# Performance work log

Measured on AMD Instinct MI355X. Metric: run time of the kernel, lower is better.

## Reference

```python
import jax, jax.numpy as jnp
import numpy as np
from jax import lax

EPS = 1e-5
F_IN, F_OUT, R = 128, 256, 16
B, H, W = 16, 128, 128


def _conv(x, w, stride):
    # x: [B,C,H,W], w: [O,I,kh,kw]; ME convs keep coordinates -> SAME padding
    return lax.conv_general_dilated(x, w, (stride, stride), 'SAME',
                                    dimension_numbers=('NCHW', 'OIHW', 'NCHW'))


def _bn(x, g, b, m, v):
    scale = g * lax.rsqrt(v + EPS)
    return x * scale[None, :, None, None] + (b - m * scale)[None, :, None, None]


def setup_inputs() -> dict:
    key = jax.random.key(0)
    ks = jax.random.split(key, 12)
    d = {}
    d['x'] = jax.random.normal(ks[0], (B, F_IN, H, W), jnp.float32)
    # BatchNorm params (eval mode running stats)
    d['bn1_g'] = jax.random.uniform(ks[1], (F_IN,), jnp.float32, 0.5, 1.5)
    d['bn1_b'] = jax.random.normal(ks[2], (F_IN,), jnp.float32) * 0.1
    d['bn1_m'] = jax.random.normal(ks[3], (F_IN,), jnp.float32) * 0.1
    d['bn1_v'] = jax.random.uniform(ks[4], (F_IN,), jnp.float32, 0.5, 1.5)
    d['bn2_g'] = jax.random.uniform(ks[5], (F_OUT,), jnp.float32, 0.5, 1.5)
    d['bn2_b'] = jax.random.normal(ks[6], (F_OUT,), jnp.float32) * 0.1
    d['bn2_m'] = jax.random.normal(ks[7], (F_OUT,), jnp.float32) * 0.1
    d['bn2_v'] = jax.random.uniform(ks[8], (F_OUT,), jnp.float32, 0.5, 1.5)
    # Conv weights (no bias, ME default)
    d['w_conv1'] = jax.random.normal(ks[9], (F_OUT, F_IN, 3, 3), jnp.float32) * (1.0 / np.sqrt(9 * F_IN))
    d['w_conv2'] = jax.random.normal(ks[10], (F_OUT, F_OUT, 3, 3), jnp.float32) * (1.0 / np.sqrt(9 * F_OUT))
    d['w_res'] = jax.random.normal(ks[11], (F_OUT, F_IN, 1, 1), jnp.float32) * (1.0 / np.sqrt(F_IN))
    # SE block linears
    k12, k13, k14, k15 = jax.random.split(jax.random.fold_in(key, 1), 4)
    d['se_w1'] = jax.random.normal(k12, (F_OUT // R, F_OUT), jnp.float32) * (1.0 / np.sqrt(F_OUT))
    d['se_b1'] = jax.random.normal(k13, (F_OUT // R,), jnp.float32) * 0.01
    d['se_w2'] = jax.random.normal(k14, (F_OUT, F_OUT // R), jnp.float32) * (1.0 / np.sqrt(F_OUT // R))
    d['se_b2'] = jax.random.normal(k15, (F_OUT,), jnp.float32) * 0.01
    return d


def reference(x, bn1_g, bn1_b, bn1_m, bn1_v, bn2_g, bn2_b, bn2_m, bn2_v,
              w_conv1, w_conv2, w_res, se_w1, se_b1, se_w2, se_b2):
    # shared BN+ReLU prefix (self.first_batch / self.first_relu reused)
    pre = jax.nn.relu(_bn(x, bn1_g, bn1_b, bn1_m, bn1_v))
    # residual branch: 1x1 stride-2 conv (f_out > f_in)
    residual = _conv(pre, w_res, 2)
    # main branch
    h = _conv(pre, w_conv1, 2)                          # [B,F_OUT,H/2,W/2]
    h = jax.nn.relu(_bn(h, bn2_g, bn2_b, bn2_m, bn2_v))
    h = _conv(h, w_conv2, 1)
    # SE attention: global avg pool -> FC -> ReLU -> FC -> sigmoid -> scale
    s = jnp.mean(h, axis=(2, 3))                        # [B,F_OUT]
    a = jax.nn.sigmoid(jax.nn.relu(s @ se_w1.T + se_b1) @ se_w2.T + se_b2)
    h = h * a[:, :, None, None]
    return h + residual
```

## Files before the change

### kernel.cpp

```cpp
#include <hip/hip_runtime.h>

typedef unsigned short u16;
typedef __attribute__((ext_vector_type(8))) unsigned short u16x8;
typedef __attribute__((ext_vector_type(8))) __bf16 bf16x8;
typedef __attribute__((ext_vector_type(4))) float f32x4;

__device__ __forceinline__ float bf2f(u16 u) {
    return __uint_as_float(((unsigned)u) << 16);
}
__device__ __forceinline__ u16 f2bf(float f) {
    unsigned u = __float_as_uint(f);
    return (u16)((u + 0x7FFFu + ((u >> 16) & 1u)) >> 16);
}

__global__ void setup_kernel(const float* __restrict__ w1, const float* __restrict__ w2,
                             const float* __restrict__ wr,
                             const float* __restrict__ g2, const float* __restrict__ b2,
                             const float* __restrict__ m2, const float* __restrict__ v2,
                             u16* __restrict__ w1t, u16* __restrict__ w2t,
                             u16* __restrict__ wrt, float* __restrict__ bias2f,
                             u16* __restrict__ pre, u16* __restrict__ h1) {
    int b = blockIdx.x;
    if (b < 3585) {
        int i = b * 256 + threadIdx.x;
        if (i < 294912) {
            int ci = i & 127; int t = i >> 7; int o = t & 255; int tap = t >> 8;
            int dy = tap / 3, dx = tap - dy * 3;
            float sc = g2[o] * rsqrtf(v2[o] + 1e-5f);
            w1t[i] = f2bf(w1[((o * 128 + ci) * 3 + dy) * 3 + dx] * sc);
        } else if (i < 294912 + 589824) {
            int j = i - 294912;
            int ci = j & 255; int t = j >> 8; int o = t & 255; int tap = t >> 8;
            int dy = tap / 3, dx = tap - dy * 3;
            w2t[j] = f2bf(w2[((o * 256 + ci) * 3 + dy) * 3 + dx]);
        } else if (i < 294912 + 589824 + 32768) {
            int j = i - (294912 + 589824);
            int ci = j & 127; int o = j >> 7;
            wrt[j] = f2bf(wr[o * 128 + ci]);
        } else {
            int o = i - (294912 + 589824 + 32768);
            if (o < 256) {
                float sc = g2[o] * rsqrtf(v2[o] + 1e-5f);
                bias2f[o] = b2[o] - m2[o] * sc;
            }
        }
    } else if (b < 3585 + 2056) {
        int i = (b - 3585) * 256 + threadIdx.x;
        if (i < 16 * 129 * 128) {
            int c = i & 127; int t = i >> 7; int n = t / 129; int xx = t - n * 129;
            pre[((n * 129 + 128) * 129 + xx) * 128 + c] = 0;
        } else {
            int j = i - 16 * 129 * 128;
            int c = j & 127; int t = j >> 7; int n = t >> 7; int y = t & 127;
            pre[((n * 129 + y) * 129 + 128) * 128 + c] = 0;
        }
    } else {
        int i = (b - (3585 + 2056)) * 256 + threadIdx.x;
        int c = i & 255;
        int t = i >> 8;
        int n = t / 260;
        int cl = t - n * 260;
        int y, x;
        if (cl < 66)       { y = 0;  x = cl; }
        else if (cl < 132) { y = 65; x = cl - 66; }
        else if (cl < 196) { x = 0;  y = cl - 131; }
        else               { x = 65; y = cl - 195; }
        h1[((n * 66 + y) * 66 + x) * 256 + c] = 0;
    }
}

__global__ void pre_kernel(const float* __restrict__ x, const float* __restrict__ g,
                           const float* __restrict__ b, const float* __restrict__ m,
                           const float* __restrict__ v, u16* __restrict__ pre) {
    __shared__ u16 tile[128 * 136];
    int n = blockIdx.x >> 7, y = blockIdx.x & 127;
    int tid = threadIdx.x;
    int c = tid >> 1, xh = (tid & 1) << 6;
    float sc = g[c] * rsqrtf(v[c] + 1e-5f);
    float bi = b[c] - m[c] * sc;
    const float4* src = (const float4*)(x + (((n * 128 + c) * 128 + y) << 7) + xh);
#pragma unroll
    for (int j = 0; j < 16; ++j) {
        float4 val = src[j];
        int xb = xh + j * 4;
        tile[(xb + 0) * 136 + c] = f2bf(fmaxf(val.x * sc + bi, 0.f));
        tile[(xb + 1) * 136 + c] = f2bf(fmaxf(val.y * sc + bi, 0.f));
        tile[(xb + 2) * 136 + c] = f2bf(fmaxf(val.z * sc + bi, 0.f));
        tile[(xb + 3) * 136 + c] = f2bf(fmaxf(val.w * sc + bi, 0.f));
    }
    __syncthreads();
    int c0 = (tid & 15) << 3;
#pragma unroll
    for (int xi = 0; xi < 8; ++xi) {
        int xx = xi * 16 + (tid >> 4);
        u16x8 val = *(const u16x8*)&tile[xx * 136 + c0];
        *(u16x8*)(pre + ((n * 129 + y) * 129 + xx) * 128 + c0) = val;
    }
}

template <int CIN, int NTAPS, int STRIDE, bool BIASRELU, bool POOL>
__global__ __launch_bounds__(512, 2)
void conv_8ph(const u16* __restrict__ in, const u16* __restrict__ wt,
              const float* __restrict__ bias, u16* __restrict__ out,
              float* __restrict__ pool_out,
              int in_row, int in_img, int out_base, int out_row, int out_img) {
    constexpr int CSTEPS = CIN / 64;
    constexpr int KT = CSTEPS * NTAPS;
    __shared__ __attribute__((aligned(16))) u16 lds[81920];

    const int tid = threadIdx.x;
    const int w = tid >> 6, l = tid & 63;
    const int wm = w >> 2, wn = w & 3;
    const int l15 = l & 15;
    const int Mbase = blockIdx.x << 8;

    const int srow = tid >> 3;
    const int swze = (((tid & 7) ^ (srow & 7)) << 3);
    int pix0 = Mbase + srow;
    int nn0 = pix0 >> 12, p0 = (pix0 >> 6) & 63, q0 = pix0 & 63;
    const int abase0 = nn0 * in_img + (STRIDE * p0) * in_row + (STRIDE * q0) * CIN + swze;
    const int astep = STRIDE * in_row;
    const int bbase0 = srow * CIN + swze;
    const int bstep = 64 * CIN;

    int colw[2];
#pragma unroll
    for (int kk = 0; kk < 2; ++kk)
        colw[kk] = (kk * 32 + (l >> 4) * 8) ^ ((l & 7) << 3);

    f32x4 acc[8][4] = {};
    bf16x8 afr[4][2], b0f[2][2], b1f[2][2];

#define AOFF(ks) (((NTAPS == 9) ? ((((ks) / CSTEPS) / 3) * in_row + (((ks) / CSTEPS) % 3) * CIN) : 0) + ((ks) % CSTEPS) * 64)
#define BOFF(ks) (((ks) / CSTEPS) * 256 * CIN + ((ks) % CSTEPS) * 64)
#define GLDS(gsrc, ldst) __builtin_amdgcn_global_load_lds(                          \
        (__attribute__((address_space(1))) void*)(gsrc),                            \
        (__attribute__((address_space(3))) void*)(ldst), 16, 0, 0)
#define STAGE_A(base, h, ks) {                                                      \
    int _ao = AOFF(ks);                                                             \
    GLDS(in + abase0 + (2 * (h) + 0) * astep + _ao,                                 \
         &lds[(base) + (h) * 8192 + 0 * 4096 + w * 512]);                           \
    GLDS(in + abase0 + (2 * (h) + 1) * astep + _ao,                                 \
         &lds[(base) + (h) * 8192 + 1 * 4096 + w * 512]); }
#define STAGE_B(base, h, ks) {                                                      \
    int _bo = BOFF(ks);                                                             \
    GLDS(wt + bbase0 + (2 * (h) + 0) * bstep + _bo,                                 \
         &lds[(base) + (h) * 8192 + 0 * 4096 + w * 512]);                           \
    GLDS(wt + bbase0 + (2 * (h) + 1) * bstep + _bo,                                 \
         &lds[(base) + (h) * 8192 + 1 * 4096 + w * 512]); }
#define BARRIER() { __builtin_amdgcn_s_barrier(); asm volatile("" ::: "memory"); }
#define LDA(base, MH) {                                                             \
    _Pragma("unroll") for (int fm = 0; fm < 4; ++fm)                                \
    _Pragma("unroll") for (int kk = 0; kk < 2; ++kk)                                \
        afr[fm][kk] = *(const bf16x8*)&lds[(base) + ((MH) * 128 + wm * 64 + fm * 16 + l15) * 64 + colw[kk]]; }
#define LDB(base, NH, dst) {                                                        \
    _Pragma("unroll") for (int gn = 0; gn < 2; ++gn)                                \
    _Pragma("unroll") for (int kk = 0; kk < 2; ++kk)                                \
        dst[gn][kk] = *(const bf16x8*)&lds[(base) + ((NH) * 128 + gn * 64 + wn * 16 + l15) * 64 + colw[kk]]; }
#define MFMA_Q(MH, NH, bset) {                                                      \
    _Pragma("unroll") for (int fm = 0; fm < 4; ++fm)                                \
    _Pragma("unroll") for (int gn = 0; gn < 2; ++gn)                                \
    _Pragma("unroll") for (int kk = 0; kk < 2; ++kk)                                \
        acc[(MH) * 4 + fm][(NH) * 2 + gn] = __builtin_amdgcn_mfma_f32_16x16x32_bf16( \
            afr[fm][kk], bset[gn][kk], acc[(MH) * 4 + fm][(NH) * 2 + gn], 0, 0, 0); }

    STAGE_A(0, 0, 0); STAGE_A(0, 1, 0);
    STAGE_B(49152, 0, 0); STAGE_B(49152, 1, 0);
    STAGE_A(16384, 0, 1); STAGE_A(16384, 1, 1);
    asm volatile("s_waitcnt vmcnt(4)" ::: "memory");
    BARRIER();

    int Ar = 0;
    int As = 32768;
    int Brel = 0;

#pragma unroll 1
    for (int t = 0; t < KT - 2; ++t) {
        const int Br = 49152 + Brel, Bs = 49152 + (Brel ^ 16384);
        LDA(Ar, 0);
        LDB(Br, 0, b0f);
        LDB(Br, 1, b1f);
        STAGE_B(Bs, 0, t + 1); STAGE_B(Bs, 1, t + 1);
        __builtin_amdgcn_s_setprio(1);
        MFMA_Q(0, 0, b0f);
        MFMA_Q(0, 1, b1f);
        __builtin_amdgcn_s_setprio(0);
        LDA(Ar, 1);
        STAGE_A(As, 0, t + 2); STAGE_A(As, 1, t + 2);
        __builtin_amdgcn_s_setprio(1);
        MFMA_Q(1, 1, b1f);
        MFMA_Q(1, 0, b0f);
        __builtin_amdgcn_s_setprio(0);
        asm volatile("s_waitcnt vmcnt(4)" ::: "memory");
        BARRIER();
        Ar = (Ar == 32768) ? 0 : Ar + 16384;
        As = (As == 32768) ? 0 : As + 16384;
        Brel ^= 16384;
    }

    {
        const int Br = 49152 + Brel, Bs = 49152 + (Brel ^ 16384);
        LDA(Ar, 0);
        LDB(Br, 0, b0f);
        LDB(Br, 1, b1f);
        STAGE_B(Bs, 0, KT - 1); STAGE_B(Bs, 1, KT - 1);
        __builtin_amdgcn_s_setprio(1);
        MFMA_Q(0, 0, b0f);
        MFMA_Q(0, 1, b1f);
        __builtin_amdgcn_s_setprio(0);
        LDA(Ar, 1);
        __builtin_amdgcn_s_setprio(1);
        MFMA_Q(1, 1, b1f);
        MFMA_Q(1, 0, b0f);
        __builtin_amdgcn_s_setprio(0);
        asm volatile("s_waitcnt vmcnt(0)" ::: "memory");
        BARRIER();
        Ar = (Ar == 32768) ? 0 : Ar + 16384;
        Brel ^= 16384;
    }
    {
        const int Br = 49152 + Brel;
        LDA(Ar, 0);
        LDB(Br, 0, b0f);
        LDB(Br, 1, b1f);
        MFMA_Q(0, 0, b0f);
        MFMA_Q(0, 1, b1f);
        LDA(Ar, 1);
        MFMA_Q(1, 1, b1f);
        MFMA_Q(1, 0, b0f);
    }
#undef AOFF
#undef BOFF
#undef GLDS
#undef STAGE_A
#undef STAGE_B
#undef LDA
#undef LDB

#pragma unroll
    for (int f = 0; f < 8; ++f) {
        const int prow = (f >> 2) * 128 + wm * 64 + (f & 3) * 16 + ((l >> 4) << 2);
#pragma unroll
        for (int g = 0; g < 4; ++g) {
            const int o = (g >> 1) * 128 + (g & 1) * 64 + wn * 16 + l15;
            float bb = 0.f;
            if (BIASRELU) bb = bias[o];
#pragma unroll
            for (int j = 0; j < 4; ++j) {
                int pix = Mbase + prow + j;
                int nn = pix >> 12, p = (pix >> 6) & 63, q = pix & 63;
                float val = acc[f][g][j] + bb;
                if (BIASRELU) val = fmaxf(val, 0.f);
                out[out_base + nn * out_img + p * out_row + q * 256 + o] = f2bf(val);
            }
        }
    }

    if (POOL) {
        float ps[4];
#pragma unroll
        for (int g = 0; g < 4; ++g) {
            float s = 0.f;
#pragma unroll
            for (int f = 0; f < 8; ++f)
#pragma unroll
                for (int j = 0; j < 4; ++j) s += acc[f][g][j];
            s += __shfl_xor(s, 16);
            s += __shfl_xor(s, 32);
            ps[g] = s;
        }
        asm volatile("s_waitcnt lgkmcnt(0)" ::: "memory");
        BARRIER();
        float* fl = (float*)lds;
        if ((l >> 4) == 0) {
#pragma unroll
            for (int g = 0; g < 4; ++g) {
                int o = (g >> 1) * 128 + (g & 1) * 64 + wn * 16 + l15;
                fl[wm * 256 + o] = ps[g];
            }
        }
        BARRIER();
        if (tid < 256)
            pool_out[blockIdx.x * 256 + tid] = fl[tid] + fl[256 + tid];
    }
#undef MFMA_Q
#undef BARRIER
}

template <int CIN, int NTAPS, int STRIDE, bool BIASRELU>
__global__ __launch_bounds__(256, 2)
void conv_mfma(const u16* __restrict__ in, const u16* __restrict__ wt,
               const float* __restrict__ bias, u16* __restrict__ out,
               int in_row, int in_img, int out_base, int out_row, int out_img) {
    constexpr int CSTEPS = CIN / 64;
    constexpr int KSTEPS = CSTEPS * NTAPS;
    __shared__ u16 lA[128 * 64];
    __shared__ u16 lB[128 * 64];

    const int tid = threadIdx.x;
    const int w = tid >> 6, l = tid & 63;
    const int bn = blockIdx.x & 1;
    const int Mbase = (blockIdx.x >> 1) << 7;
    const int wm = w >> 1, wn = w & 1;
    const int srow = l >> 3;
    const int chunk = l & 7;

    int abase[4], wbase[4];
#pragma unroll
    for (int i = 0; i < 4; ++i) {
        int pix = w * 32 + i * 8 + srow;
        int mm = Mbase + pix;
        int nn = mm >> 12, p = (mm >> 6) & 63, q = mm & 63;
        abase[i] = nn * in_img + (STRIDE * p) * in_row + (STRIDE * q) * CIN + chunk * 8;
        wbase[i] = (bn * 128 + pix) * CIN + chunk * 8;
    }

    f32x4 acc[4][4] = {};

    int abyte[4], bbyte[4];
#pragma unroll
    for (int f = 0; f < 4; ++f) {
        abyte[f] = ((wm * 64 + f * 16 + (l & 15)) * 64 + ((l >> 4) * 8)) * 2;
        bbyte[f] = ((wn * 64 + f * 16 + (l & 15)) * 64 + ((l >> 4) * 8)) * 2;
    }

    for (int ks = 0; ks < KSTEPS; ++ks) {
        const int tap = ks / CSTEPS;
        const int c0 = (ks % CSTEPS) * 64;
        const int dy = (NTAPS == 9) ? (tap / 3) : 0;
        const int dx = (NTAPS == 9) ? (tap - dy * 3) : 0;
        const int aoff = dy * in_row + dx * CIN + c0;
        const int boff = tap * 256 * CIN + c0;
        __syncthreads();
#pragma unroll
        for (int i = 0; i < 4; ++i) {
            const u16* gsrc = in + abase[i] + aoff;
            u16* ldst = &lA[(w * 32 + i * 8) * 64];
            __builtin_amdgcn_global_load_lds((__attribute__((address_space(1))) void*)gsrc,
                                             (__attribute__((address_space(3))) void*)ldst,
                                             16, 0, 0);
        }
#pragma unroll
        for (int i = 0; i < 4; ++i) {
            const u16* gsrc = wt + wbase[i] + boff;
            u16* ldst = &lB[(w * 32 + i * 8) * 64];
            __builtin_amdgcn_global_load_lds((__attribute__((address_space(1))) void*)gsrc,
                                             (__attribute__((address_space(3))) void*)ldst,
                                             16, 0, 0);
        }
        __syncthreads();
#pragma unroll
        for (int kk = 0; kk < 2; ++kk) {
            bf16x8 af[4], bv[4];
#pragma unroll
            for (int f = 0; f < 4; ++f)
                af[f] = *(const bf16x8*)((const char*)lA + abyte[f] + kk * 64);
#pragma unroll
            for (int f = 0; f < 4; ++f)
                bv[f] = *(const bf16x8*)((const char*)lB + bbyte[f] + kk * 64);
#pragma unroll
            for (int fm = 0; fm < 4; ++fm)
#pragma unroll
                for (int fn = 0; fn < 4; ++fn)
                    acc[fm][fn] = __builtin_amdgcn_mfma_f32_16x16x32_bf16(
                        af[fm], bv[fn], acc[fm][fn], 0, 0, 0);
        }
    }

#pragma unroll
    for (int fm = 0; fm < 4; ++fm) {
        const int mloc = wm * 64 + fm * 16 + ((l >> 4) << 2);
#pragma unroll
        for (int fn = 0; fn < 4; ++fn) {
            const int o = bn * 128 + wn * 64 + fn * 16 + (l & 15);
            float bb = 0.f;
            if (BIASRELU) bb = bias[o];
#pragma unroll
            for (int j = 0; j < 4; ++j) {
                int mm = Mbase + mloc + j;
                int nn = mm >> 12, p = (mm >> 6) & 63, q = mm & 63;
                float val = acc[fm][fn][j] + bb;
                if (BIASRELU) val = fmaxf(val, 0.f);
                out[out_base + nn * out_img + p * out_row + q * 256 + o] = f2bf(val);
            }
        }
    }
}

__global__ void se_kernel(const float* __restrict__ partial,
                          const float* __restrict__ w1, const float* __restrict__ b1,
                          const float* __restrict__ w2, const float* __restrict__ b2,
                          float* __restrict__ a) {
    __shared__ float sm[16 * 256];
    __shared__ float hl[16 * 16];
    int t = threadIdx.x;
    for (int n = 0; n < 16; ++n) {
        float s = 0.f;
#pragma unroll
        for (int k = 0; k < 16; ++k) s += partial[(n * 16 + k) * 256 + t];
        sm[n * 256 + t] = s * (1.0f / 4096.0f);
    }
    __syncthreads();
    {
        int bb = t >> 4, j = t & 15;
        float d = b1[j];
        for (int c = 0; c < 256; ++c) d += sm[bb * 256 + c] * w1[j * 256 + c];
        hl[bb * 16 + j] = fmaxf(d, 0.f);
    }
    __syncthreads();
    {
        int o = t;
        for (int bb = 0; bb < 16; ++bb) {
            float z = b2[o];
            for (int j = 0; j < 16; ++j) z += hl[bb * 16 + j] * w2[o * 16 + j];
            a[bb * 256 + o] = 1.0f / (1.0f + expf(-z));
        }
    }
}

__global__ void finalize_kernel(const u16* __restrict__ h2, const u16* __restrict__ res,
                                const float* __restrict__ a, float* __restrict__ out) {
    __shared__ u16 th[256 * 68];
    __shared__ float al[256];
    int n = blockIdx.x >> 6, p = blockIdx.x & 63;
    int t = threadIdx.x;
    al[t] = a[n * 256 + t];
    __syncthreads();
    int o8 = (t & 31) << 3, qr = t >> 5;
    int pixbase = n * 4096 + p * 64;
#pragma unroll
    for (int qi = 0; qi < 8; ++qi) {
        int q = qi * 8 + qr;
        int gi = (pixbase + q) * 256 + o8;
        u16x8 hv = *(const u16x8*)(h2 + gi);
        u16x8 rv = *(const u16x8*)(res + gi);
#pragma unroll
        for (int k = 0; k < 8; ++k) {
            float vv = bf2f(hv[k]) * al[o8 + k] + bf2f(rv[k]);
            th[(o8 + k) * 68 + q] = f2bf(vv);
        }
    }
    __syncthreads();
    int q4 = (t & 15) << 2, ob = t >> 4;
#pragma unroll
    for (int oi = 0; oi < 16; ++oi) {
        int o = oi * 16 + ob;
        float4 vv;
        vv.x = bf2f(th[o * 68 + q4 + 0]);
        vv.y = bf2f(th[o * 68 + q4 + 1]);
        vv.z = bf2f(th[o * 68 + q4 + 2]);
        vv.w = bf2f(th[o * 68 + q4 + 3]);
        *(float4*)(out + ((n * 256 + o) * 64 + p) * 64 + q4) = vv;
    }
}

static const size_t OFF_PRE  = 0;
static const size_t OFF_H1   = 68161536;
static const size_t OFF_RES  = 103845888;
static const size_t OFF_W1T  = 137400320;
static const size_t OFF_W2T  = 137990144;
static const size_t OFF_WRT  = 139169792;
static const size_t OFF_B2F  = 139235328;
static const size_t OFF_PART = 139236352;
static const size_t OFF_A    = 139760640;

extern "C" void kernel_launch(void* const* d_in, const int* in_sizes, int n_in,
                              void* d_out, int out_size, void* d_ws, size_t ws_size,
                              hipStream_t stream) {
    (void)in_sizes; (void)n_in; (void)out_size; (void)ws_size;
    const float* x      = (const float*)d_in[0];
    const float* bn1_g  = (const float*)d_in[1];
    const float* bn1_b  = (const float*)d_in[2];
    const float* bn1_m  = (const float*)d_in[3];
    const float* bn1_v  = (const float*)d_in[4];
    const float* bn2_g  = (const float*)d_in[5];
    const float* bn2_b  = (const float*)d_in[6];
    const float* bn2_m  = (const float*)d_in[7];
    const float* bn2_v  = (const float*)d_in[8];
    const float* wc1    = (const float*)d_in[9];
    const float* wc2    = (const float*)d_in[10];
    const float* wres   = (const float*)d_in[11];
    const float* se_w1  = (const float*)d_in[12];
    const float* se_b1  = (const float*)d_in[13];
    const float* se_w2  = (const float*)d_in[14];
    const float* se_b2  = (const float*)d_in[15];

    char* ws = (char*)d_ws;
    u16*   pre    = (u16*)(ws + OFF_PRE);
    u16*   h2     = (u16*)(ws + OFF_PRE);
    u16*   h1     = (u16*)(ws + OFF_H1);
    u16*   res    = (u16*)(ws + OFF_RES);
    u16*   w1t    = (u16*)(ws + OFF_W1T);
    u16*   w2t    = (u16*)(ws + OFF_W2T);
    u16*   wrt    = (u16*)(ws + OFF_WRT);
    float* bias2f = (float*)(ws + OFF_B2F);
    float* part   = (float*)(ws + OFF_PART);
    float* avec   = (float*)(ws + OFF_A);
    float* out    = (float*)d_out;

    setup_kernel<<<9801, 256, 0, stream>>>(wc1, wc2, wres, bn2_g, bn2_b, bn2_m, bn2_v,
                                           w1t, w2t, wrt, bias2f, pre, h1);
    pre_kernel<<<2048, 256, 0, stream>>>(x, bn1_g, bn1_b, bn1_m, bn1_v, pre);

    conv_8ph<128, 9, 2, true, false><<<256, 512, 0, stream>>>(
        pre, w1t, bias2f, h1, nullptr,
        129 * 128, 129 * 129 * 128,
        67 * 256, 66 * 256, 66 * 66 * 256);

    conv_mfma<128, 1, 2, false><<<1024, 256, 0, stream>>>(
        pre, wrt, nullptr, res,
        129 * 128, 129 * 129 * 128,
        0, 64 * 256, 4096 * 256);

    conv_8ph<256, 9, 1, false, true><<<256, 512, 0, stream>>>(
        h1, w2t, nullptr, h2, part,
        66 * 256, 66 * 66 * 256,
        0, 64 * 256, 4096 * 256);

    se_kernel<<<1, 256, 0, stream>>>(part, se_w1, se_b1, se_w2, se_b2, avec);
    finalize_kernel<<<1024, 256, 0, stream>>>(h2, res, avec, out);
}
```

Before: 212.9 us.

## Software-pipeline B fragment loads, swizzle block order, reuse 8-phase conv for residual

Result: no change. 209.3 us (-1.7%).

```diff
diff --git a/kernel.cpp b/kernel.cpp
--- a/kernel.cpp
+++ b/kernel.cpp
@@ -112,7 +112,8 @@
     const int w = tid >> 6, l = tid & 63;
     const int wm = w >> 2, wn = w & 3;
     const int l15 = l & 15;
-    const int Mbase = blockIdx.x << 8;
+    const int bid = ((blockIdx.x & 7) << 5) | (blockIdx.x >> 3);
+    const int Mbase = bid << 8;
 
     const int srow = tid >> 3;
     const int swze = (((tid & 7) ^ (srow & 7)) << 3);
@@ -129,7 +130,7 @@
         colw[kk] = (kk * 32 + (l >> 4) * 8) ^ ((l & 7) << 3);
 
     f32x4 acc[8][4] = {};
-    bf16x8 afr[4][2], b0f[2][2], b1f[2][2];
+    bf16x8 afr[4][2], bXf[2][2], bYf[2][2];
 
 #define AOFF(ks) (((NTAPS == 9) ? ((((ks) / CSTEPS) / 3) * in_row + (((ks) / CSTEPS) % 3) * CIN) : 0) + ((ks) % CSTEPS) * 64)
 #define BOFF(ks) (((ks) / CSTEPS) * 256 * CIN + ((ks) % CSTEPS) * 64)
@@ -174,61 +175,53 @@
     int As = 32768;
     int Brel = 0;
 
+    LDB(49152, 0, bXf);
+
+#define CBODY(T, B0, B1, STAGEA, VM)                                                \
+    {                                                                               \
+        const int Br = 49152 + Brel, Bs = 49152 + (Brel ^ 16384);                   \
+        LDA(Ar, 0);                                                                 \
+        LDB(Br, 1, B1);                                                             \
+        STAGE_B(Bs, 0, (T) + 1); STAGE_B(Bs, 1, (T) + 1);                           \
+        __builtin_amdgcn_s_setprio(1);                                              \
+        MFMA_Q(0, 0, B0);                                                           \
+        MFMA_Q(0, 1, B1);                                                           \
+        __builtin_amdgcn_s_setprio(0);                                              \
+        LDA(Ar, 1);                                                                 \
+        if (STAGEA) { STAGE_A(As, 0, (T) + 2); STAGE_A(As, 1, (T) + 2); }           \
+        __builtin_amdgcn_s_setprio(1);                                              \
+        MFMA_Q(1, 1, B1);                                                           \
+        __builtin_amdgcn_s_setprio(0);                                              \
+        asm volatile("s_waitcnt vmcnt(" #VM ")" ::: "memory");                      \
+        BARRIER();                                                                  \
+        LDB(49152 + (Brel ^ 16384), 0, B1);         \
+        __builtin_amdgcn_s_setprio(1);                                              \
+        MFMA_Q(1, 0, B0);                                   \
+        __builtin_amdgcn_s_setprio(0);                                              \
+        Ar = (Ar == 32768) ? 0 : Ar + 16384;                                        \
+        As = (As == 32768) ? 0 : As + 16384;                                        \
+        Brel ^= 16384;                                                              \
+    }
+
 #pragma unroll 1
-    for (int t = 0; t < KT - 2; ++t) {
-        const int Br = 49152 + Brel, Bs = 49152 + (Brel ^ 16384);
-        LDA(Ar, 0);
-        LDB(Br, 0, b0f);
-        LDB(Br, 1, b1f);
-        STAGE_B(Bs, 0, t + 1); STAGE_B(Bs, 1, t + 1);
-        __builtin_amdgcn_s_setprio(1);
-        MFMA_Q(0, 0, b0f);
-        MFMA_Q(0, 1, b1f);
-        __builtin_amdgcn_s_setprio(0);
-        LDA(Ar, 1);
-        STAGE_A(As, 0, t + 2); STAGE_A(As, 1, t + 2);
-        __builtin_amdgcn_s_setprio(1);
-        MFMA_Q(1, 1, b1f);
-        MFMA_Q(1, 0, b0f);
-        __builtin_amdgcn_s_setprio(0);
-        asm volatile("s_waitcnt vmcnt(4)" ::: "memory");
-        BARRIER();
-        Ar = (Ar == 32768) ? 0 : Ar + 16384;
-        As = (As == 32768) ? 0 : As + 16384;
-        Brel ^= 16384;
-    }
-
-    {
-        const int Br = 49152 + Brel, Bs = 49152 + (Brel ^ 16384);
-        LDA(Ar, 0);
-        LDB(Br, 0, b0f);
-        LDB(Br, 1, b1f);
-        STAGE_B(Bs, 0, KT - 1); STAGE_B(Bs, 1, KT - 1);
-        __builtin_amdgcn_s_setprio(1);
-        MFMA_Q(0, 0, b0f);
-        MFMA_Q(0, 1, b1f);
-        __builtin_amdgcn_s_setprio(0);
-        LDA(Ar, 1);
-        __builtin_amdgcn_s_setprio(1);
-        MFMA_Q(1, 1, b1f);
-        MFMA_Q(1, 0, b0f);
-        __builtin_amdgcn_s_setprio(0);
-        asm volatile("s_waitcnt vmcnt(0)" ::: "memory");
-        BARRIER();
-        Ar = (Ar == 32768) ? 0 : Ar + 16384;
-        Brel ^= 16384;
-    }
+    for (int t = 0; t < KT - 2; t += 2) {
+        CBODY(t,     bXf, bYf, true, 4);
+        CBODY(t + 1, bYf, bXf, true, 4);
+    }
+
+    CBODY(KT - 2, bXf, bYf, false, 0);
+
     {
         const int Br = 49152 + Brel;
         LDA(Ar, 0);
-        LDB(Br, 0, b0f);
-        LDB(Br, 1, b1f);
-        MFMA_Q(0, 0, b0f);
-        MFMA_Q(0, 1, b1f);
+        LDB(Br, 1, bXf);
+        MFMA_Q(0, 0, bYf);
+        MFMA_Q(0, 1, bXf);
         LDA(Ar, 1);
-        MFMA_Q(1, 1, b1f);
-        MFMA_Q(1, 0, b0f);
-    }
+        MFMA_Q(1, 1, bXf);
+        MFMA_Q(1, 0, bYf);
+    }
+#undef CBODY
 #undef AOFF
 #undef BOFF
 #undef GLDS
@@ -281,110 +274,10 @@
         }
         BARRIER();
         if (tid < 256)
-            pool_out[blockIdx.x * 256 + tid] = fl[tid] + fl[256 + tid];
+            pool_out[bid * 256 + tid] = fl[tid] + fl[256 + tid];
     }
 #undef MFMA_Q
 #undef BARRIER
-}
-
-template <int CIN, int NTAPS, int STRIDE, bool BIASRELU>
-__global__ __launch_bounds__(256, 2)
-void conv_mfma(const u16* __restrict__ in, const u16* __restrict__ wt,
-               const float* __restrict__ bias, u16* __restrict__ out,
-               int in_row, int in_img, int out_base, int out_row, int out_img) {
-    constexpr int CSTEPS = CIN / 64;
-    constexpr int KSTEPS = CSTEPS * NTAPS;
-    __shared__ u16 lA[128 * 64];
-    __shared__ u16 lB[128 * 64];
-
-    const int tid = threadIdx.x;
-    const int w = tid >> 6, l = tid & 63;
-    const int bn = blockIdx.x & 1;
-    const int Mbase = (blockIdx.x >> 1) << 7;
-    const int wm = w >> 1, wn = w & 1;
-    const int srow = l >> 3;
-    const int chunk = l & 7;
-
-    int abase[4], wbase[4];
-#pragma unroll
-    for (int i = 0; i < 4; ++i) {
-        int pix = w * 32 + i * 8 + srow;
-        int mm = Mbase + pix;
-        int nn = mm >> 12, p = (mm >> 6) & 63, q = mm & 63;
-        abase[i] = nn * in_img + (STRIDE * p) * in_row + (STRIDE * q) * CIN + chunk * 8;
-        wbase[i] = (bn * 128 + pix) * CIN + chunk * 8;
-    }
-
-    f32x4 acc[4][4] = {};
-
-    int abyte[4], bbyte[4];
-#pragma unroll
-    for (int f = 0; f < 4; ++f) {
-        abyte[f] = ((wm * 64 + f * 16 + (l & 15)) * 64 + ((l >> 4) * 8)) * 2;
-        bbyte[f] = ((wn * 64 + f * 16 + (l & 15)) * 64 + ((l >> 4) * 8)) * 2;
-    }
-
-    for (int ks = 0; ks < KSTEPS; ++ks) {
-        const int tap = ks / CSTEPS;
-        const int c0 = (ks % CSTEPS) * 64;
-        const int dy = (NTAPS == 9) ? (tap / 3) : 0;
-        const int dx = (NTAPS == 9) ? (tap - dy * 3) : 0;
-        const int aoff = dy * in_row + dx * CIN + c0;
-        const int boff = tap * 256 * CIN + c0;
-        __syncthreads();
-#pragma unroll
-        for (int i = 0; i < 4; ++i) {
-            const u16* gsrc = in + abase[i] + aoff;
-            u16* ldst = &lA[(w * 32 + i * 8) * 64];
-            __builtin_amdgcn_global_load_lds((__attribute__((address_space(1))) void*)gsrc,
-                                             (__attribute__((address_space(3))) void*)ldst,
-                                             16, 0, 0);
-        }
-#pragma unroll
-        for (int i = 0; i < 4; ++i) {
-            const u16* gsrc = wt + wbase[i] + boff;
-            u16* ldst = &lB[(w * 32 + i * 8) * 64];
-            __builtin_amdgcn_global_load_lds((__attribute__((address_space(1))) void*)gsrc,
-                                             (__attribute__((address_space(3))) void*)ldst,
-                                             16, 0, 0);
-        }
-        __syncthreads();
-#pragma unroll
-        for (int kk = 0; kk < 2; ++kk) {
-            bf16x8 af[4], bv[4];
-#pragma unroll
-            for (int f = 0; f < 4; ++f)
-                af[f] = *(const bf16x8*)((const char*)lA + abyte[f] + kk * 64);
-#pragma unroll
-            for (int f = 0; f < 4; ++f)
-                bv[f] = *(const bf16x8*)((const char*)lB + bbyte[f] + kk * 64);
-#pragma unroll
-            for (int fm = 0; fm < 4; ++fm)
-#pragma unroll
-                for (int fn = 0; fn < 4; ++fn)
-                    acc[fm][fn] = __builtin_amdgcn_mfma_f32_16x16x32_bf16(
-                        af[fm], bv[fn], acc[fm][fn], 0, 0, 0);
-        }
-    }
-
-#pragma unroll
-    for (int fm = 0; fm < 4; ++fm) {
-        const int mloc = wm * 64 + fm * 16 + ((l >> 4) << 2);
-#pragma unroll
-        for (int fn = 0; fn < 4; ++fn) {
-            const int o = bn * 128 + wn * 64 + fn * 16 + (l & 15);
-            float bb = 0.f;
-            if (BIASRELU) bb = bias[o];
-#pragma unroll
-            for (int j = 0; j < 4; ++j) {
-                int mm = Mbase + mloc + j;
-                int nn = mm >> 12, p = (mm >> 6) & 63, q = mm & 63;
-                float val = acc[fm][fn][j] + bb;
-                if (BIASRELU) val = fmaxf(val, 0.f);
-                out[out_base + nn * out_img + p * out_row + q * 256 + o] = f2bf(val);
-            }
-        }
-    }
 }
 
 __global__ void se_kernel(const float* __restrict__ partial,
@@ -507,8 +400,8 @@
         129 * 128, 129 * 129 * 128,
         67 * 256, 66 * 256, 66 * 66 * 256);
 
-    conv_mfma<128, 1, 2, false><<<1024, 256, 0, stream>>>(
-        pre, wrt, nullptr, res,
+    conv_8ph<128, 1, 2, false, false><<<256, 512, 0, stream>>>(
+        pre, wrt, nullptr, res, nullptr,
         129 * 128, 129 * 129 * 128,
         0, 64 * 256, 4096 * 256);
 
```
